# Kernel tuning notes

Measured on AMD Instinct MI355X. Metric: run time of the kernel, lower is better.

The kernel has to match this reference:

```python
import jax, jax.numpy as jnp
import numpy as np

B, N, E = 4, 4096, 65536
DIN, DB, DO, T = 128, 64, 128, 4  # in_features, bond_features, out_features, n_edge_types
DCAT = 2 * DIN + DB


def setup_inputs() -> dict:
    key = jax.random.key(0)
    ks = jax.random.split(key, 24)
    s = 0.05
    inp = {
        "sites": jax.random.normal(ks[0], (B, N, DIN), jnp.float32),
        "bonds": jax.random.normal(ks[1], (B, E, DB), jnp.float32),
        "idx1": jax.random.randint(ks[2], (E,), 0, N),
        "idx2": jax.random.randint(ks[3], (E,), 0, N),
        "uc": jax.random.randint(ks[4], (E,), 0, T),
        # per-type 2-layer MLPs (stacked over types)
        "W1a": jax.random.normal(ks[5], (T, DCAT, DO), jnp.float32) * s,
        "b1a": jnp.zeros((T, DO), jnp.float32),
        "W1b": jax.random.normal(ks[6], (T, DO, DO), jnp.float32) * s,
        "b1b": jnp.zeros((T, DO), jnp.float32),
        "W2a": jax.random.normal(ks[7], (T, DCAT, DO), jnp.float32) * s,
        "b2a": jnp.zeros((T, DO), jnp.float32),
        "W2b": jax.random.normal(ks[8], (T, DO, DO), jnp.float32) * s,
        "b2b": jnp.zeros((T, DO), jnp.float32),
        # attention gates (Linear(out,1) + sigmoid)
        "Wa1": jax.random.normal(ks[9], (DO, 1), jnp.float32) * s,
        "ba1": jnp.zeros((1,), jnp.float32),
        "Wa2": jax.random.normal(ks[10], (DO, 1), jnp.float32) * s,
        "ba2": jnp.zeros((1,), jnp.float32),
    }
    return inp


def reference(sites, bonds, idx1, idx2, uc, W1a, b1a, W1b, b1b,
              W2a, b2a, W2b, b2b, Wa1, ba1, Wa2, ba2):
    lrelu = jax.nn.leaky_relu  # negative_slope 0.01, matches nn.LeakyReLU default
    # gather edge endpoints and concat with bond features: [B, E, 2*DIN+DB]
    v = jnp.concatenate([sites[:, idx1], sites[:, idx2], bonds], axis=2)

    def mlp(Wa, ba, Wb, bb):
        return lrelu(v @ Wa + ba) @ Wb + bb  # [B, E, DO]

    n_types = W1a.shape[0]
    out1 = jnp.zeros((v.shape[0], v.shape[1], W1b.shape[-1]), v.dtype)
    out2 = jnp.zeros_like(out1)
    for i in range(n_types):  # small fixed set of structurally distinct weights
        m = (uc == i)[None, :, None]
        out1 = jnp.where(m, mlp(W1a[i], b1a[i], W1b[i], b1b[i]), out1)
        out2 = jnp.where(m, mlp(W2a[i], b2a[i], W2b[i], b2b[i]), out2)
    out1 = lrelu(out1)
    out2 = lrelu(out2)
    # sigmoid attention gate
    g1 = jax.nn.sigmoid(out1 @ Wa1 + ba1) * out1
    g2 = jax.nn.sigmoid(out2 @ Wa2 + ba2) * out2
    # scatter_add over edges -> nodes along dim 1, then sum
    n_nodes = sites.shape[1]
    agg = jnp.zeros((sites.shape[0], n_nodes, out1.shape[-1]), v.dtype)
    agg = agg.at[:, idx2].add(g1 + g2)
    return agg
```

## Files before the change

### kernel.cpp

```cpp
#include <hip/hip_runtime.h>

#define NB 4
#define NN 4096
#define NE 65536
#define DIN 128
#define DB 64
#define DOUT 128
#define NT 4
#define DCAT 320

#define MT 64
#define LDH (DOUT + 8)

typedef __bf16 bf16;
typedef __bf16 bf16x2 __attribute__((ext_vector_type(2)));
typedef __bf16 bf16x4 __attribute__((ext_vector_type(4)));
typedef __bf16 bf16x8 __attribute__((ext_vector_type(8)));
typedef float floatx4 __attribute__((ext_vector_type(4)));

__device__ __forceinline__ void async16(const void* g, void* l) {
    __builtin_amdgcn_global_load_lds(
        (const __attribute__((address_space(1))) unsigned int*)g,
        (__attribute__((address_space(3))) unsigned int*)l, 16, 0, 0);
}

#define NS4 (NB * NN * DIN / 4)
#define NA  (NT * 256 * DCAT)
#define NB2 (NT * 256 * DOUT)
#define NBO4 (NB * NE * DB / 4)
#define NZERO 8208
__global__ void prep_k(const float* __restrict__ sites, const float* __restrict__ bonds,
                       const float* __restrict__ W1a, const float* __restrict__ W2a,
                       const float* __restrict__ W1b, const float* __restrict__ W2b,
                       bf16* __restrict__ sitesB,
                       bf16* __restrict__ WtA, bf16* __restrict__ WtB,
                       bf16* __restrict__ bondsB,
                       int* __restrict__ zeroRegion) {
    int i = blockIdx.x * 256 + threadIdx.x;
    if (i < NZERO) zeroRegion[i] = 0;
    if (i < NS4) {
        float4 f = ((const float4*)sites)[i];
        bf16x4 h = { (bf16)f.x, (bf16)f.y, (bf16)f.z, (bf16)f.w };
        ((bf16x4*)sitesB)[i] = h;
    } else if (i < NS4 + NA) {
        int j = i - NS4;
        int k = j % DCAT;
        int n = (j / DCAT) % 256;
        int t = j / (DCAT * 256);
        float w = (n < DOUT) ? W1a[(t * DCAT + k) * DOUT + n]
                             : W2a[(t * DCAT + k) * DOUT + (n - DOUT)];
        WtA[j] = (bf16)w;
    } else if (i < NS4 + NA + NB2) {
        int j = i - NS4 - NA;
        int k = j % DOUT;
        int n = (j / DOUT) % 256;
        int t = j / (DOUT * 256);
        float w = (n < DOUT) ? W1b[(t * DOUT + k) * DOUT + n]
                             : W2b[(t * DOUT + k) * DOUT + (n - DOUT)];
        WtB[j] = (bf16)w;
    } else {
        int j = i - NS4 - NA - NB2;
        float4 f = ((const float4*)bonds)[j];
        bf16x4 h = { (bf16)f.x, (bf16)f.y, (bf16)f.z, (bf16)f.w };
        ((bf16x4*)bondsB)[j] = h;
    }
}

__global__ void bucket_k(const int* __restrict__ uc, const int* __restrict__ idx2,
                         int* __restrict__ cnt, int* __restrict__ deg,
                         int* __restrict__ bucket) {
    __shared__ int h[NT];
    __shared__ int baseo[NT];
    int tid = threadIdx.x;
    if (tid < NT) h[tid] = 0;
    __syncthreads();
    int e = blockIdx.x * 256 + tid;
    int t = uc[e] & 3;
    int lp = atomicAdd(&h[t], 1);
    __syncthreads();
    if (tid < NT) baseo[tid] = atomicAdd(&cnt[tid], h[tid]);
    __syncthreads();
    bucket[t * NE + baseo[t] + lp] = e;
    atomicAdd(&deg[idx2[e] & (NN - 1)], 1);
}

__global__ void scan_k(const int* __restrict__ deg, int* __restrict__ off) {
    __shared__ int wsum[4];
    int tid = threadIdx.x;
    int lane = tid & 63, w = tid >> 6;
    int v[16]; int s = 0;
    #pragma unroll
    for (int j = 0; j < 16; ++j) { v[j] = deg[tid * 16 + j]; s += v[j]; }
    int inc = s;
    #pragma unroll
    for (int d = 1; d < 64; d <<= 1) {
        int x = __shfl_up(inc, d, 64);
        if (lane >= d) inc += x;
    }
    if (lane == 63) wsum[w] = inc;
    __syncthreads();
    int wpre = 0;
    #pragma unroll
    for (int j = 0; j < 4; ++j) wpre += (j < w) ? wsum[j] : 0;
    int excl = wpre + inc - s;
    #pragma unroll
    for (int j = 0; j < 16; ++j) { off[tid * 16 + j] = excl; excl += v[j]; }
    if (tid == 255) off[4096] = excl;
}

__global__ void fill_k(const int* __restrict__ idx2, const int* __restrict__ off,
                       int* __restrict__ cursor, int* __restrict__ perm) {
    int e = blockIdx.x * 256 + threadIdx.x;
    int n = idx2[e] & (NN - 1);
    int p = atomicAdd(&cursor[n], 1);
    perm[e] = off[n] + p;
}

__launch_bounds__(256, 4)
__global__ void main_k(const bf16* __restrict__ sitesB, const bf16* __restrict__ bondsB,
                       const int* __restrict__ idx1, const int* __restrict__ idx2,
                       const int* __restrict__ cnt, const int* __restrict__ bucket,
                       const int* __restrict__ perm,
                       const bf16* __restrict__ WtA, const bf16* __restrict__ WtB,
                       const float* __restrict__ b1a, const float* __restrict__ b2a,
                       const float* __restrict__ b1b, const float* __restrict__ b2b,
                       const float* __restrict__ Wa1, const float* __restrict__ ba1,
                       const float* __restrict__ Wa2, const float* __restrict__ ba2,
                       bf16* __restrict__ eo) {
    __shared__ __align__(16) char smem[40960];
    bf16* sA  = (bf16*)smem;
    bf16* sB  = (bf16*)(smem + 8192);
    bf16* sH1 = (bf16*)smem;
    bf16* sH2 = (bf16*)(smem + MT * LDH * 2);
    float* sWa = (float*)(smem + 35840);

    const int tid = threadIdx.x;

    int blk = blockIdx.x;
    int p = blk & 7;
    const int b = p >> 1;
    int flat = ((blk >> 3) << 1) + (p & 1);

    int c0 = cnt[0], c1 = cnt[1], c2 = cnt[2], c3 = cnt[3];
    int n0 = (c0 + MT - 1) / MT, n1 = (c1 + MT - 1) / MT,
        n2 = (c2 + MT - 1) / MT, n3 = (c3 + MT - 1) / MT;
    int t, ti, cT;
    if (flat < n0)                { t = 0; ti = flat;                cT = c0; }
    else if (flat < n0+n1)        { t = 1; ti = flat - n0;           cT = c1; }
    else if (flat < n0+n1+n2)     { t = 2; ti = flat - n0 - n1;      cT = c2; }
    else if (flat < n0+n1+n2+n3)  { t = 3; ti = flat - n0 - n1 - n2; cT = c3; }
    else return;
    const int base = ti * MT;
    const int nvalid = min(MT, cT - base);

    const int rowA = tid >> 2;
    const int rr = min(rowA, max(nvalid - 1, 0));
    const int e  = bucket[t * NE + base + rr] & (NE - 1);
    const int r1 = idx1[e] & (NN - 1);
    const int r2 = idx2[e] & (NN - 1);
    const int prm = perm[e] & (NE - 1);

    const int wv = tid >> 6;
    const int lane = tid & 63;
    const int br = wv >> 1;
    const int nh = wv & 1;
    const int lr = lane & 15;
    const int quad = lane >> 4;
    const int lk = quad * 8;
    const int colbase = nh * 64;
    const int lodd = lane & 1;

    const size_t sbase = (size_t)b * NN;
    const int kseg = (tid & 3) ^ (rowA & 3);
    const bf16* pA1 = sitesB + (sbase + r1) * DIN + kseg * 8;
    const bf16* pA2 = sitesB + (sbase + r2) * DIN + kseg * 8;
    const bf16* pBo = bondsB + ((size_t)b * NE + e) * DB + kseg * 8;

    auto stageA = [&](int ks, int buf) {
        const bf16* src = (ks < 4) ? (pA1 + ks * 32)
                        : (ks < 8) ? (pA2 + (ks - 4) * 32)
                                   : (pBo + (ks - 8) * 32);
        async16(src, smem + buf * 4096 + wv * 1024);
    };
    auto stageB1 = [&](int ks, int buf) {
        #pragma unroll
        for (int j = 0; j < 4; ++j) {
            int d = (j * 4 + wv) * 64 + lane;
            int col = d >> 2;
            int ksg = (d & 3) ^ (col & 3);
            const bf16* src = WtA + (size_t)(t * 256 + col) * DCAT + ks * 32 + ksg * 8;
            async16(src, &sB[buf * 8192 + (j * 4 + wv) * 512]);
        }
    };

    floatx4 acc[4][4];
    #pragma unroll
    for (int mt = 0; mt < 4; ++mt)
        #pragma unroll
        for (int nt = 0; nt < 4; ++nt)
            acc[mt][nt] = (floatx4){0.f, 0.f, 0.f, 0.f};

    stageA(0, 0);
    stageB1(0, 0);
    #pragma unroll
    for (int ks = 0; ks < 10; ++ks) {
        int buf = ks & 1;
        __syncthreads();
        if (ks < 9) {
            stageA(ks + 1, buf ^ 1);
            stageB1(ks + 1, buf ^ 1);
        }
        bf16x8 aF[4];
        #pragma unroll
        for (int mt = 0; mt < 4; ++mt) {
            int row = mt * 16 + lr;
            aF[mt] = *(const bf16x8*)(&sA[buf * 2048 + (row * 4 + (quad ^ (lr & 3))) * 8]);
        }
        #pragma unroll
        for (int nt = 0; nt < 4; ++nt) {
            int cc = br * 128 + colbase + nt * 16 + lr;
            bf16x8 bF = *(const bf16x8*)(&sB[buf * 8192 + (cc * 4 + (quad ^ (lr & 3))) * 8]);
            #pragma unroll
            for (int mt = 0; mt < 4; ++mt)
                acc[mt][nt] = __builtin_amdgcn_mfma_f32_16x16x32_bf16(aF[mt], bF, acc[mt][nt], 0, 0, 0);
        }
    }
    __syncthreads();

    sWa[tid] = (tid < 128) ? Wa1[tid] : Wa2[tid - 128];

    bf16* sH = (br == 0) ? sH1 : sH2;
    const float* biasA = ((br == 0) ? b1a : b2a) + t * DOUT;
    #pragma unroll
    for (int nt = 0; nt < 4; ++nt) {
        int c = colbase + nt * 16 + lr;
        int cpair = c & ~1;
        float bias = biasA[c];
        #pragma unroll
        for (int mt = 0; mt < 4; ++mt) {
            float v[4], x[4];
            #pragma unroll
            for (int rg = 0; rg < 4; ++rg) {
                float u = acc[mt][nt][rg] + bias;
                v[rg] = u > 0.f ? u : 0.01f * u;
            }
            #pragma unroll
            for (int rg = 0; rg < 4; ++rg) x[rg] = __shfl_xor(v[rg], 1);
            int r0 = mt * 16 + quad * 4 + lodd * 2;
            float lo0 = lodd ? x[2] : v[0], hi0 = lodd ? v[2] : x[0];
            float lo1 = lodd ? x[3] : v[1], hi1 = lodd ? v[3] : x[1];
            *(bf16x2*)(&sH[r0 * LDH + cpair])       = (bf16x2){ (bf16)lo0, (bf16)hi0 };
            *(bf16x2*)(&sH[(r0 + 1) * LDH + cpair]) = (bf16x2){ (bf16)lo1, (bf16)hi1 };
        }
    }
    __syncthreads();

    floatx4 acc2[4][4];
    #pragma unroll
    for (int mt = 0; mt < 4; ++mt)
        #pragma unroll
        for (int nt = 0; nt < 4; ++nt)
            acc2[mt][nt] = (floatx4){0.f, 0.f, 0.f, 0.f};

    const bf16* sHa = (br == 0) ? sH1 : sH2;
    const bf16* WtB_w = WtB + (size_t)(t * 256 + br * 128 + colbase) * DOUT + lk;
    #pragma unroll
    for (int ks = 0; ks < 4; ++ks) {
        bf16x8 aF[4];
        #pragma unroll
        for (int mt = 0; mt < 4; ++mt)
            aF[mt] = *(const bf16x8*)(&sHa[(mt * 16 + lr) * LDH + ks * 32 + lk]);
        #pragma unroll
        for (int nt = 0; nt < 4; ++nt) {
            bf16x8 bF = *(const bf16x8*)(&WtB_w[(size_t)(nt * 16 + lr) * DOUT + ks * 32]);
            #pragma unroll
            for (int mt = 0; mt < 4; ++mt)
                acc2[mt][nt] = __builtin_amdgcn_mfma_f32_16x16x32_bf16(aF[mt], bF, acc2[mt][nt], 0, 0, 0);
        }
    }
    __syncthreads();

    const float* biasB = ((br == 0) ? b1b : b2b) + t * DOUT;
    #pragma unroll
    for (int nt = 0; nt < 4; ++nt) {
        int c = colbase + nt * 16 + lr;
        int cpair = c & ~1;
        float bias = biasB[c];
        #pragma unroll
        for (int mt = 0; mt < 4; ++mt) {
            float v[4], x[4];
            #pragma unroll
            for (int rg = 0; rg < 4; ++rg) {
                float u = acc2[mt][nt][rg] + bias;
                v[rg] = u > 0.f ? u : 0.01f * u;
            }
            #pragma unroll
            for (int rg = 0; rg < 4; ++rg) x[rg] = __shfl_xor(v[rg], 1);
            int r0 = mt * 16 + quad * 4 + lodd * 2;
            float lo0 = lodd ? x[2] : v[0], hi0 = lodd ? v[2] : x[0];
            float lo1 = lodd ? x[3] : v[1], hi1 = lodd ? v[3] : x[1];
            *(bf16x2*)(&sH[r0 * LDH + cpair])       = (bf16x2){ (bf16)lo0, (bf16)hi0 };
            *(bf16x2*)(&sH[(r0 + 1) * LDH + cpair]) = (bf16x2){ (bf16)lo1, (bf16)hi1 };
        }
    }
    __syncthreads();

    {
        int m = tid >> 2;
        int q = tid & 3;
        float d1 = 0.f, d2 = 0.f;
        #pragma unroll
        for (int j = 0; j < 4; ++j) {
            bf16x8 h1 = *(const bf16x8*)(&sH1[m * LDH + q * 32 + j * 8]);
            bf16x8 h2 = *(const bf16x8*)(&sH2[m * LDH + q * 32 + j * 8]);
            float4 wa = *(const float4*)(&sWa[q * 32 + j * 8]);
            float4 wb = *(const float4*)(&sWa[q * 32 + j * 8 + 4]);
            float4 va = *(const float4*)(&sWa[128 + q * 32 + j * 8]);
            float4 vb = *(const float4*)(&sWa[128 + q * 32 + j * 8 + 4]);
            d1 += (float)h1[0] * wa.x; d1 += (float)h1[1] * wa.y;
            d1 += (float)h1[2] * wa.z; d1 += (float)h1[3] * wa.w;
            d1 += (float)h1[4] * wb.x; d1 += (float)h1[5] * wb.y;
            d1 += (float)h1[6] * wb.z; d1 += (float)h1[7] * wb.w;
            d2 += (float)h2[0] * va.x; d2 += (float)h2[1] * va.y;
            d2 += (float)h2[2] * va.z; d2 += (float)h2[3] * va.w;
            d2 += (float)h2[4] * vb.x; d2 += (float)h2[5] * vb.y;
            d2 += (float)h2[6] * vb.z; d2 += (float)h2[7] * vb.w;
        }
        d1 += __shfl_xor(d1, 1); d1 += __shfl_xor(d1, 2);
        d2 += __shfl_xor(d2, 1); d2 += __shfl_xor(d2, 2);
        d1 = fminf(fmaxf(d1 + ba1[0], -30.f), 30.f);
        d2 = fminf(fmaxf(d2 + ba2[0], -30.f), 30.f);
        float s1 = 1.f / (1.f + __expf(-d1));
        float s2 = 1.f / (1.f + __expf(-d2));
        if (m < nvalid) {
            bf16* dst = eo + ((size_t)b * NE + prm) * DOUT;
            #pragma unroll
            for (int j = 0; j < 4; ++j) {
                int cc = (q + 4 * j) * 8;
                bf16x8 h1 = *(const bf16x8*)(&sH1[m * LDH + cc]);
                bf16x8 h2 = *(const bf16x8*)(&sH2[m * LDH + cc]);
                bf16x8 w;
                #pragma unroll
                for (int c = 0; c < 8; ++c)
                    w[c] = (bf16)(s1 * (float)h1[c] + s2 * (float)h2[c]);
                *(bf16x8*)(dst + cc) = w;
            }
        }
    }
}

__global__ void gather_k(const bf16* __restrict__ eo, const int* __restrict__ off,
                         float* __restrict__ out) {
    __shared__ float part[16 * 128];
    int tid = threadIdx.x;
    int g = tid >> 4;
    int cseg = tid & 15;
    int n = blockIdx.x;
    int b = blockIdx.y;
    int o0 = off[n], o1 = off[n + 1];
    const bf16* base = eo + (size_t)b * NE * DOUT + cseg * 8;
    float a[8] = {0.f, 0.f, 0.f, 0.f, 0.f, 0.f, 0.f, 0.f};
    for (int r = o0 + g; r < o1; r += 16) {
        bf16x8 v = *(const bf16x8*)(base + (size_t)r * DOUT);
        #pragma unroll
        for (int j = 0; j < 8; ++j) a[j] += (float)v[j];
    }
    #pragma unroll
    for (int j = 0; j < 8; ++j) part[g * 128 + cseg * 8 + j] = a[j];
    __syncthreads();
    if (tid < 128) {
        float s = 0.f;
        #pragma unroll
        for (int g2 = 0; g2 < 16; ++g2) s += part[g2 * 128 + tid];
        out[((size_t)b * NN + n) * DOUT + tid] = s;
    }
}

extern "C" void kernel_launch(void* const* d_in, const int* in_sizes, int n_in,
                              void* d_out, int out_size, void* d_ws, size_t ws_size,
                              hipStream_t stream) {
    const float* sites = (const float*)d_in[0];
    const float* bonds = (const float*)d_in[1];
    const int*   idx1  = (const int*)d_in[2];
    const int*   idx2  = (const int*)d_in[3];
    const int*   uc    = (const int*)d_in[4];
    const float* W1a = (const float*)d_in[5];
    const float* b1a = (const float*)d_in[6];
    const float* W1b = (const float*)d_in[7];
    const float* b1b = (const float*)d_in[8];
    const float* W2a = (const float*)d_in[9];
    const float* b2a = (const float*)d_in[10];
    const float* W2b = (const float*)d_in[11];
    const float* b2b = (const float*)d_in[12];
    const float* Wa1 = (const float*)d_in[13];
    const float* ba1 = (const float*)d_in[14];
    const float* Wa2 = (const float*)d_in[15];
    const float* ba2 = (const float*)d_in[16];
    float* out = (float*)d_out;

    char* ws = (char*)d_ws;
    size_t o_cnt    = 0;
    size_t o_deg    = 64;
    size_t o_cursor = o_deg + NN * 4;
    size_t o_off    = o_cursor + NN * 4;
    size_t o_bucket = o_off + (NN + 16) * 4;
    size_t o_perm   = o_bucket + (size_t)NT * NE * 4;
    size_t o_wta    = o_perm + (size_t)NE * 4;
    size_t o_wtb    = o_wta + (size_t)NA * 2;
    size_t o_sitesB = o_wtb + (size_t)NB2 * 2;
    size_t o_eo     = o_sitesB + (size_t)NB * NN * DIN * 2;
    size_t need     = o_eo + (size_t)NB * NE * DOUT * 2;
    size_t o_bondsB = need;
    size_t need_full = o_bondsB + (size_t)NB * NE * DB * 2;
    if (ws_size < need_full) return;

    int*  cnt    = (int*)(ws + o_cnt);
    int*  deg    = (int*)(ws + o_deg);
    int*  cursor = (int*)(ws + o_cursor);
    int*  off    = (int*)(ws + o_off);
    int*  bucket = (int*)(ws + o_bucket);
    int*  perm   = (int*)(ws + o_perm);
    bf16* WtA    = (bf16*)(ws + o_wta);
    bf16* WtB    = (bf16*)(ws + o_wtb);
    bf16* sitesB = (bf16*)(ws + o_sitesB);
    bf16* eo     = (bf16*)(ws + o_eo);
    bf16* bondsB = (bf16*)(ws + o_bondsB);

    prep_k<<<(NS4 + NA + NB2 + NBO4) / 256, 256, 0, stream>>>(
        sites, bonds, W1a, W2a, W1b, W2b, sitesB, WtA, WtB, bondsB, (int*)ws);
    bucket_k<<<NE / 256, 256, 0, stream>>>(uc, idx2, cnt, deg, bucket);
    scan_k<<<1, 256, 0, stream>>>(deg, off);
    fill_k<<<NE / 256, 256, 0, stream>>>(idx2, off, cursor, perm);

    const int maxTiles = NE / MT + NT;
    main_k<<<maxTiles * NB, 256, 0, stream>>>(
        sitesB, bondsB, idx1, idx2, cnt, bucket, perm, WtA, WtB,
        b1a, b2a, b1b, b2b, Wa1, ba1, Wa2, ba2, eo);

    gather_k<<<dim3(NN, NB), 256, 0, stream>>>(eo, off, out);
}
```

Baseline: 279.7 us.

## Split main kernel tile across 8 waves with 512-thread blocks

Result: slower. 344.2 us (+23.0%).

```diff
diff --git a/kernel.cpp b/kernel.cpp
--- a/kernel.cpp
+++ b/kernel.cpp
@@ -116,7 +116,7 @@
     perm[e] = off[n] + p;
 }
 
-__launch_bounds__(256, 4)
+__launch_bounds__(512, 8)
 __global__ void main_k(const bf16* __restrict__ sitesB, const bf16* __restrict__ bondsB,
                        const int* __restrict__ idx1, const int* __restrict__ idx2,
                        const int* __restrict__ cnt, const int* __restrict__ bucket,
@@ -154,15 +154,20 @@
     const int nvalid = min(MT, cT - base);
 
     const int rowA = tid >> 2;
-    const int rr = min(rowA, max(nvalid - 1, 0));
-    const int e  = bucket[t * NE + base + rr] & (NE - 1);
-    const int r1 = idx1[e] & (NN - 1);
-    const int r2 = idx2[e] & (NN - 1);
-    const int prm = perm[e] & (NE - 1);
+    const int rrA = min(rowA, max(nvalid - 1, 0));
+    const int eA  = bucket[t * NE + base + rrA] & (NE - 1);
+    const int r1 = idx1[eA] & (NN - 1);
+    const int r2 = idx2[eA] & (NN - 1);
+
+    const int mG  = tid >> 3;
+    const int rrG = min(mG, max(nvalid - 1, 0));
+    const int eG  = bucket[t * NE + base + rrG] & (NE - 1);
+    const int prm = perm[eG] & (NE - 1);
 
     const int wv = tid >> 6;
     const int lane = tid & 63;
-    const int br = wv >> 1;
+    const int rh = wv >> 2;
+    const int br = (wv >> 1) & 1;
     const int nh = wv & 1;
     const int lr = lane & 15;
     const int quad = lane >> 4;
@@ -174,28 +179,30 @@
     const int kseg = (tid & 3) ^ (rowA & 3);
     const bf16* pA1 = sitesB + (sbase + r1) * DIN + kseg * 8;
     const bf16* pA2 = sitesB + (sbase + r2) * DIN + kseg * 8;
-    const bf16* pBo = bondsB + ((size_t)b * NE + e) * DB + kseg * 8;
+    const bf16* pBo = bondsB + ((size_t)b * NE + eA) * DB + kseg * 8;
 
     auto stageA = [&](int ks, int buf) {
-        const bf16* src = (ks < 4) ? (pA1 + ks * 32)
-                        : (ks < 8) ? (pA2 + (ks - 4) * 32)
-                                   : (pBo + (ks - 8) * 32);
-        async16(src, smem + buf * 4096 + wv * 1024);
+        if (wv < 4) {
+            const bf16* src = (ks < 4) ? (pA1 + ks * 32)
+                            : (ks < 8) ? (pA2 + (ks - 4) * 32)
+                                       : (pBo + (ks - 8) * 32);
+            async16(src, smem + buf * 4096 + wv * 1024);
+        }
     };
     auto stageB1 = [&](int ks, int buf) {
         #pragma unroll
-        for (int j = 0; j < 4; ++j) {
-            int d = (j * 4 + wv) * 64 + lane;
+        for (int j = 0; j < 2; ++j) {
+            int d = (j * 8 + wv) * 64 + lane;
             int col = d >> 2;
             int ksg = (d & 3) ^ (col & 3);
             const bf16* src = WtA + (size_t)(t * 256 + col) * DCAT + ks * 32 + ksg * 8;
-            async16(src, &sB[buf * 8192 + (j * 4 + wv) * 512]);
+            async16(src, &sB[buf * 8192 + (j * 8 + wv) * 512]);
         }
     };
 
-    floatx4 acc[4][4];
-    #pragma unroll
-    for (int mt = 0; mt < 4; ++mt)
+    floatx4 acc[2][4];
+    #pragma unroll
+    for (int mt = 0; mt < 2; ++mt)
         #pragma unroll
         for (int nt = 0; nt < 4; ++nt)
             acc[mt][nt] = (floatx4){0.f, 0.f, 0.f, 0.f};
@@ -210,10 +217,10 @@
             stageA(ks + 1, buf ^ 1);
             stageB1(ks + 1, buf ^ 1);
         }
-        bf16x8 aF[4];
-        #pragma unroll
-        for (int mt = 0; mt < 4; ++mt) {
-            int row = mt * 16 + lr;
+        bf16x8 aF[2];
+        #pragma unroll
+        for (int mt = 0; mt < 2; ++mt) {
+            int row = rh * 32 + mt * 16 + lr;
             aF[mt] = *(const bf16x8*)(&sA[buf * 2048 + (row * 4 + (quad ^ (lr & 3))) * 8]);
         }
         #pragma unroll
@@ -221,13 +228,13 @@
             int cc = br * 128 + colbase + nt * 16 + lr;
             bf16x8 bF = *(const bf16x8*)(&sB[buf * 8192 + (cc * 4 + (quad ^ (lr & 3))) * 8]);
             #pragma unroll
-            for (int mt = 0; mt < 4; ++mt)
+            for (int mt = 0; mt < 2; ++mt)
                 acc[mt][nt] = __builtin_amdgcn_mfma_f32_16x16x32_bf16(aF[mt], bF, acc[mt][nt], 0, 0, 0);
         }
     }
     __syncthreads();
 
-    sWa[tid] = (tid < 128) ? Wa1[tid] : Wa2[tid - 128];
+    if (tid < 256) sWa[tid] = (tid < 128) ? Wa1[tid] : Wa2[tid - 128];
 
     bf16* sH = (br == 0) ? sH1 : sH2;
     const float* biasA = ((br == 0) ? b1a : b2a) + t * DOUT;
@@ -237,7 +244,7 @@
         int cpair = c & ~1;
         float bias = biasA[c];
         #pragma unroll
-        for (int mt = 0; mt < 4; ++mt) {
+        for (int mt = 0; mt < 2; ++mt) {
             float v[4], x[4];
             #pragma unroll
             for (int rg = 0; rg < 4; ++rg) {
@@ -246,7 +253,7 @@
             }
             #pragma unroll
             for (int rg = 0; rg < 4; ++rg) x[rg] = __shfl_xor(v[rg], 1);
-            int r0 = mt * 16 + quad * 4 + lodd * 2;
+            int r0 = rh * 32 + mt * 16 + quad * 4 + lodd * 2;
             float lo0 = lodd ? x[2] : v[0], hi0 = lodd ? v[2] : x[0];
             float lo1 = lodd ? x[3] : v[1], hi1 = lodd ? v[3] : x[1];
             *(bf16x2*)(&sH[r0 * LDH + cpair])       = (bf16x2){ (bf16)lo0, (bf16)hi0 };
@@ -255,9 +262,9 @@
     }
     __syncthreads();
 
-    floatx4 acc2[4][4];
-    #pragma unroll
-    for (int mt = 0; mt < 4; ++mt)
+    floatx4 acc2[2][4];
+    #pragma unroll
+    for (int mt = 0; mt < 2; ++mt)
         #pragma unroll
         for (int nt = 0; nt < 4; ++nt)
             acc2[mt][nt] = (floatx4){0.f, 0.f, 0.f, 0.f};
@@ -266,15 +273,15 @@
     const bf16* WtB_w = WtB + (size_t)(t * 256 + br * 128 + colbase) * DOUT + lk;
     #pragma unroll
     for (int ks = 0; ks < 4; ++ks) {
-        bf16x8 aF[4];
-        #pragma unroll
-        for (int mt = 0; mt < 4; ++mt)
-            aF[mt] = *(const bf16x8*)(&sHa[(mt * 16 + lr) * LDH + ks * 32 + lk]);
+        bf16x8 aF[2];
+        #pragma unroll
+        for (int mt = 0; mt < 2; ++mt)
+            aF[mt] = *(const bf16x8*)(&sHa[(rh * 32 + mt * 16 + lr) * LDH + ks * 32 + lk]);
         #pragma unroll
         for (int nt = 0; nt < 4; ++nt) {
             bf16x8 bF = *(const bf16x8*)(&WtB_w[(size_t)(nt * 16 + lr) * DOUT + ks * 32]);
             #pragma unroll
-            for (int mt = 0; mt < 4; ++mt)
+            for (int mt = 0; mt < 2; ++mt)
                 acc2[mt][nt] = __builtin_amdgcn_mfma_f32_16x16x32_bf16(aF[mt], bF, acc2[mt][nt], 0, 0, 0);
         }
     }
@@ -287,7 +294,7 @@
         int cpair = c & ~1;
         float bias = biasB[c];
         #pragma unroll
-        for (int mt = 0; mt < 4; ++mt) {
+        for (int mt = 0; mt < 2; ++mt) {
             float v[4], x[4];
             #pragma unroll
             for (int rg = 0; rg < 4; ++rg) {
@@ -296,7 +303,7 @@
             }
             #pragma unroll
             for (int rg = 0; rg < 4; ++rg) x[rg] = __shfl_xor(v[rg], 1);
-            int r0 = mt * 16 + quad * 4 + lodd * 2;
+            int r0 = rh * 32 + mt * 16 + quad * 4 + lodd * 2;
             float lo0 = lodd ? x[2] : v[0], hi0 = lodd ? v[2] : x[0];
             float lo1 = lodd ? x[3] : v[1], hi1 = lodd ? v[3] : x[1];
             *(bf16x2*)(&sH[r0 * LDH + cpair])       = (bf16x2){ (bf16)lo0, (bf16)hi0 };
@@ -306,17 +313,17 @@
     __syncthreads();
 
     {
-        int m = tid >> 2;
-        int q = tid & 3;
+        int m = mG;
+        int qq = tid & 7;
         float d1 = 0.f, d2 = 0.f;
         #pragma unroll
-        for (int j = 0; j < 4; ++j) {
-            bf16x8 h1 = *(const bf16x8*)(&sH1[m * LDH + q * 32 + j * 8]);
-            bf16x8 h2 = *(const bf16x8*)(&sH2[m * LDH + q * 32 + j * 8]);
-            float4 wa = *(const float4*)(&sWa[q * 32 + j * 8]);
-            float4 wb = *(const float4*)(&sWa[q * 32 + j * 8 + 4]);
-            float4 va = *(const float4*)(&sWa[128 + q * 32 + j * 8]);
-            float4 vb = *(const float4*)(&sWa[128 + q * 32 + j * 8 + 4]);
+        for (int j = 0; j < 2; ++j) {
+            bf16x8 h1 = *(const bf16x8*)(&sH1[m * LDH + qq * 16 + j * 8]);
+            bf16x8 h2 = *(const bf16x8*)(&sH2[m * LDH + qq * 16 + j * 8]);
+            float4 wa = *(const float4*)(&sWa[qq * 16 + j * 8]);
+            float4 wb = *(const float4*)(&sWa[qq * 16 + j * 8 + 4]);
+            float4 va = *(const float4*)(&sWa[128 + qq * 16 + j * 8]);
+            float4 vb = *(const float4*)(&sWa[128 + qq * 16 + j * 8 + 4]);
             d1 += (float)h1[0] * wa.x; d1 += (float)h1[1] * wa.y;
             d1 += (float)h1[2] * wa.z; d1 += (float)h1[3] * wa.w;
             d1 += (float)h1[4] * wb.x; d1 += (float)h1[5] * wb.y;
@@ -326,24 +333,23 @@
             d2 += (float)h2[4] * vb.x; d2 += (float)h2[5] * vb.y;
             d2 += (float)h2[6] * vb.z; d2 += (float)h2[7] * vb.w;
         }
-        d1 += __shfl_xor(d1, 1); d1 += __shfl_xor(d1, 2);
-        d2 += __shfl_xor(d2, 1); d2 += __shfl_xor(d2, 2);
+        d1 += __shfl_xor(d1, 1); d1 += __shfl_xor(d1, 2); d1 += __shfl_xor(d1, 4);
+        d2 += __shfl_xor(d2, 1); d2 += __shfl_xor(d2, 2); d2 += __shfl_xor(d2, 4);
         d1 = fminf(fmaxf(d1 + ba1[0], -30.f), 30.f);
         d2 = fminf(fmaxf(d2 + ba2[0], -30.f), 30.f);
         float s1 = 1.f / (1.f + __expf(-d1));
         float s2 = 1.f / (1.f + __expf(-d2));
         if (m < nvalid) {
-            bf16* dst = eo + ((size_t)b * NE + prm) * DOUT;
-            #pragma unroll
-            for (int j = 0; j < 4; ++j) {
-                int cc = (q + 4 * j) * 8;
-                bf16x8 h1 = *(const bf16x8*)(&sH1[m * LDH + cc]);
-                bf16x8 h2 = *(const bf16x8*)(&sH2[m * LDH + cc]);
+            bf16* dst = eo + ((size_t)b * NE + prm) * DOUT + qq * 16;
+            #pragma unroll
+            for (int j = 0; j < 2; ++j) {
+                bf16x8 h1 = *(const bf16x8*)(&sH1[m * LDH + qq * 16 + j * 8]);
+                bf16x8 h2 = *(const bf16x8*)(&sH2[m * LDH + qq * 16 + j * 8]);
                 bf16x8 w;
                 #pragma unroll
                 for (int c = 0; c < 8; ++c)
                     w[c] = (bf16)(s1 * (float)h1[c] + s2 * (float)h2[c]);
-                *(bf16x8*)(dst + cc) = w;
+                *(bf16x8*)(dst + j * 8) = w;
             }
         }
     }
@@ -433,7 +439,7 @@
     fill_k<<<NE / 256, 256, 0, stream>>>(idx2, off, cursor, perm);
 
     const int maxTiles = NE / MT + NT;
-    main_k<<<maxTiles * NB, 256, 0, stream>>>(
+    main_k<<<maxTiles * NB, 512, 0, stream>>>(
         sitesB, bondsB, idx1, idx2, cnt, bucket, perm, WtA, WtB,
         b1a, b2a, b1b, b2b, Wa1, ba1, Wa2, ba2, eo);
 
```

## Load first-layer MFMA operands directly from global memory instead of LDS staging

Applied to the files above, without the earlier changes.

Result: slower. 401.3 us (+43.5%).

```diff
diff --git a/kernel.cpp b/kernel.cpp
--- a/kernel.cpp
+++ b/kernel.cpp
@@ -17,12 +17,6 @@
 typedef __bf16 bf16x4 __attribute__((ext_vector_type(4)));
 typedef __bf16 bf16x8 __attribute__((ext_vector_type(8)));
 typedef float floatx4 __attribute__((ext_vector_type(4)));
-
-__device__ __forceinline__ void async16(const void* g, void* l) {
-    __builtin_amdgcn_global_load_lds(
-        (const __attribute__((address_space(1))) unsigned int*)g,
-        (__attribute__((address_space(3))) unsigned int*)l, 16, 0, 0);
-}
 
 #define NS4 (NB * NN * DIN / 4)
 #define NA  (NT * 256 * DCAT)
@@ -127,12 +121,12 @@
                        const float* __restrict__ Wa1, const float* __restrict__ ba1,
                        const float* __restrict__ Wa2, const float* __restrict__ ba2,
                        bf16* __restrict__ eo) {
-    __shared__ __align__(16) char smem[40960];
-    bf16* sA  = (bf16*)smem;
-    bf16* sB  = (bf16*)(smem + 8192);
+    __shared__ __align__(16) char smem[35584];
     bf16* sH1 = (bf16*)smem;
     bf16* sH2 = (bf16*)(smem + MT * LDH * 2);
-    float* sWa = (float*)(smem + 35840);
+    int* sI1  = (int*)(smem + 34816);
+    int* sI2  = (int*)(smem + 35072);
+    int* sEid = (int*)(smem + 35328);
 
     const int tid = threadIdx.x;
 
@@ -153,12 +147,19 @@
     const int base = ti * MT;
     const int nvalid = min(MT, cT - base);
 
-    const int rowA = tid >> 2;
-    const int rr = min(rowA, max(nvalid - 1, 0));
-    const int e  = bucket[t * NE + base + rr] & (NE - 1);
-    const int r1 = idx1[e] & (NN - 1);
-    const int r2 = idx2[e] & (NN - 1);
-    const int prm = perm[e] & (NE - 1);
+    const int mG  = tid >> 2;
+    const int rrG = min(mG, max(nvalid - 1, 0));
+    const int eG  = bucket[t * NE + base + rrG] & (NE - 1);
+    const int prm = perm[eG] & (NE - 1);
+
+    if (tid < MT) {
+        int rr = min(tid, max(nvalid - 1, 0));
+        int e = bucket[t * NE + base + rr] & (NE - 1);
+        sEid[tid] = e;
+        sI1[tid] = idx1[e] & (NN - 1);
+        sI2[tid] = idx2[e] & (NN - 1);
+    }
+    __syncthreads();
 
     const int wv = tid >> 6;
     const int lane = tid & 63;
@@ -170,28 +171,20 @@
     const int colbase = nh * 64;
     const int lodd = lane & 1;
 
-    const size_t sbase = (size_t)b * NN;
-    const int kseg = (tid & 3) ^ (rowA & 3);
-    const bf16* pA1 = sitesB + (sbase + r1) * DIN + kseg * 8;
-    const bf16* pA2 = sitesB + (sbase + r2) * DIN + kseg * 8;
-    const bf16* pBo = bondsB + ((size_t)b * NE + e) * DB + kseg * 8;
-
-    auto stageA = [&](int ks, int buf) {
-        const bf16* src = (ks < 4) ? (pA1 + ks * 32)
-                        : (ks < 8) ? (pA2 + (ks - 4) * 32)
-                                   : (pBo + (ks - 8) * 32);
-        async16(src, smem + buf * 4096 + wv * 1024);
-    };
-    auto stageB1 = [&](int ks, int buf) {
-        #pragma unroll
-        for (int j = 0; j < 4; ++j) {
-            int d = (j * 4 + wv) * 64 + lane;
-            int col = d >> 2;
-            int ksg = (d & 3) ^ (col & 3);
-            const bf16* src = WtA + (size_t)(t * 256 + col) * DCAT + ks * 32 + ksg * 8;
-            async16(src, &sB[buf * 8192 + (j * 4 + wv) * 512]);
-        }
-    };
+    const unsigned sbase = (unsigned)b * NN;
+    unsigned oA1[4], oA2[4], oBo[4], oB[4];
+    #pragma unroll
+    for (int mt = 0; mt < 4; ++mt) {
+        int rw = mt * 16 + lr;
+        oA1[mt] = (sbase + (unsigned)sI1[rw]) * DIN + lk;
+        oA2[mt] = (sbase + (unsigned)sI2[rw]) * DIN + lk;
+        oBo[mt] = ((unsigned)b * NE + (unsigned)sEid[rw]) * DB + lk;
+    }
+    #pragma unroll
+    for (int nt = 0; nt < 4; ++nt) {
+        int cc = br * 128 + colbase + nt * 16 + lr;
+        oB[nt] = ((unsigned)t * 256 + (unsigned)cc) * DCAT + lk;
+    }
 
     floatx4 acc[4][4];
     #pragma unroll
@@ -200,34 +193,24 @@
         for (int nt = 0; nt < 4; ++nt)
             acc[mt][nt] = (floatx4){0.f, 0.f, 0.f, 0.f};
 
-    stageA(0, 0);
-    stageB1(0, 0);
     #pragma unroll
     for (int ks = 0; ks < 10; ++ks) {
-        int buf = ks & 1;
-        __syncthreads();
-        if (ks < 9) {
-            stageA(ks + 1, buf ^ 1);
-            stageB1(ks + 1, buf ^ 1);
-        }
-        bf16x8 aF[4];
+        bf16x8 aF[4], bF[4];
         #pragma unroll
         for (int mt = 0; mt < 4; ++mt) {
-            int row = mt * 16 + lr;
-            aF[mt] = *(const bf16x8*)(&sA[buf * 2048 + (row * 4 + (quad ^ (lr & 3))) * 8]);
-        }
-        #pragma unroll
-        for (int nt = 0; nt < 4; ++nt) {
-            int cc = br * 128 + colbase + nt * 16 + lr;
-            bf16x8 bF = *(const bf16x8*)(&sB[buf * 8192 + (cc * 4 + (quad ^ (lr & 3))) * 8]);
+            aF[mt] = (ks < 4) ? *(const bf16x8*)(sitesB + oA1[mt] + ks * 32)
+                   : (ks < 8) ? *(const bf16x8*)(sitesB + oA2[mt] + (ks - 4) * 32)
+                              : *(const bf16x8*)(bondsB + oBo[mt] + (ks - 8) * 32);
+        }
+        #pragma unroll
+        for (int nt = 0; nt < 4; ++nt)
+            bF[nt] = *(const bf16x8*)(WtA + oB[nt] + ks * 32);
+        #pragma unroll
+        for (int nt = 0; nt < 4; ++nt)
             #pragma unroll
             for (int mt = 0; mt < 4; ++mt)
-                acc[mt][nt] = __builtin_amdgcn_mfma_f32_16x16x32_bf16(aF[mt], bF, acc[mt][nt], 0, 0, 0);
-        }
-    }
-    __syncthreads();
-
-    sWa[tid] = (tid < 128) ? Wa1[tid] : Wa2[tid - 128];
+                acc[mt][nt] = __builtin_amdgcn_mfma_f32_16x16x32_bf16(aF[mt], bF[nt], acc[mt][nt], 0, 0, 0);
+    }
 
     bf16* sH = (br == 0) ? sH1 : sH2;
     const float* biasA = ((br == 0) ? b1a : b2a) + t * DOUT;
@@ -306,17 +289,17 @@
     __syncthreads();
 
     {
-        int m = tid >> 2;
+        int m = mG;
         int q = tid & 3;
         float d1 = 0.f, d2 = 0.f;
         #pragma unroll
         for (int j = 0; j < 4; ++j) {
             bf16x8 h1 = *(const bf16x8*)(&sH1[m * LDH + q * 32 + j * 8]);
             bf16x8 h2 = *(const bf16x8*)(&sH2[m * LDH + q * 32 + j * 8]);
-            float4 wa = *(const float4*)(&sWa[q * 32 + j * 8]);
-            float4 wb = *(const float4*)(&sWa[q * 32 + j * 8 + 4]);
-            float4 va = *(const float4*)(&sWa[128 + q * 32 + j * 8]);
-            float4 vb = *(const float4*)(&sWa[128 + q * 32 + j * 8 + 4]);
+            float4 wa = *(const float4*)(&Wa1[q * 32 + j * 8]);
+            float4 wb = *(const float4*)(&Wa1[q * 32 + j * 8 + 4]);
+            float4 va = *(const float4*)(&Wa2[q * 32 + j * 8]);
+            float4 vb = *(const float4*)(&Wa2[q * 32 + j * 8 + 4]);
             d1 += (float)h1[0] * wa.x; d1 += (float)h1[1] * wa.y;
             d1 += (float)h1[2] * wa.z; d1 += (float)h1[3] * wa.w;
             d1 += (float)h1[4] * wb.x; d1 += (float)h1[5] * wb.y;
```

## Merge bucketing into prep, assign scatter slots in main kernel, pack gather nodes

Applied to the files above, without the earlier changes.

New measurement: 269.0 us. 1.04x faster.

```diff
diff --git a/kernel.cpp b/kernel.cpp
--- a/kernel.cpp
+++ b/kernel.cpp
@@ -28,16 +28,33 @@
 #define NA  (NT * 256 * DCAT)
 #define NB2 (NT * 256 * DOUT)
 #define NBO4 (NB * NE * DB / 4)
-#define NZERO 8208
+#define PREP_BLOCKS ((NS4 + NA + NB2 + NBO4) / 256)
 __global__ void prep_k(const float* __restrict__ sites, const float* __restrict__ bonds,
                        const float* __restrict__ W1a, const float* __restrict__ W2a,
                        const float* __restrict__ W1b, const float* __restrict__ W2b,
+                       const int* __restrict__ uc, const int* __restrict__ idx2,
                        bf16* __restrict__ sitesB,
                        bf16* __restrict__ WtA, bf16* __restrict__ WtB,
                        bf16* __restrict__ bondsB,
-                       int* __restrict__ zeroRegion) {
-    int i = blockIdx.x * 256 + threadIdx.x;
-    if (i < NZERO) zeroRegion[i] = 0;
+                       int* __restrict__ cnt, int* __restrict__ deg,
+                       int* __restrict__ bucket) {
+    int tid = threadIdx.x;
+    if (blockIdx.x < 256) {
+        __shared__ int h[NT];
+        __shared__ int baseo[NT];
+        if (tid < NT) h[tid] = 0;
+        __syncthreads();
+        int e = blockIdx.x * 256 + tid;
+        int t = uc[e] & 3;
+        int lp = atomicAdd(&h[t], 1);
+        __syncthreads();
+        if (tid < NT) baseo[tid] = atomicAdd(&cnt[tid], h[tid]);
+        __syncthreads();
+        bucket[t * NE + baseo[t] + lp] = e;
+        atomicAdd(&deg[idx2[e] & (NN - 1)], 1);
+        return;
+    }
+    int i = (blockIdx.x - 256) * 256 + tid;
     if (i < NS4) {
         float4 f = ((const float4*)sites)[i];
         bf16x4 h = { (bf16)f.x, (bf16)f.y, (bf16)f.z, (bf16)f.w };
@@ -66,27 +83,12 @@
     }
 }
 
-__global__ void bucket_k(const int* __restrict__ uc, const int* __restrict__ idx2,
-                         int* __restrict__ cnt, int* __restrict__ deg,
-                         int* __restrict__ bucket) {
-    __shared__ int h[NT];
-    __shared__ int baseo[NT];
-    int tid = threadIdx.x;
-    if (tid < NT) h[tid] = 0;
-    __syncthreads();
-    int e = blockIdx.x * 256 + tid;
-    int t = uc[e] & 3;
-    int lp = atomicAdd(&h[t], 1);
-    __syncthreads();
-    if (tid < NT) baseo[tid] = atomicAdd(&cnt[tid], h[tid]);
-    __syncthreads();
-    bucket[t * NE + baseo[t] + lp] = e;
-    atomicAdd(&deg[idx2[e] & (NN - 1)], 1);
-}
-
-__global__ void scan_k(const int* __restrict__ deg, int* __restrict__ off) {
+__global__ void scan_k(const int* __restrict__ deg, int* __restrict__ off,
+                       int* __restrict__ cursor) {
     __shared__ int wsum[4];
     int tid = threadIdx.x;
+    #pragma unroll
+    for (int j = 0; j < NB * NN / 256; ++j) cursor[tid + j * 256] = 0;
     int lane = tid & 63, w = tid >> 6;
     int v[16]; int s = 0;
     #pragma unroll
@@ -106,21 +108,13 @@
     #pragma unroll
     for (int j = 0; j < 16; ++j) { off[tid * 16 + j] = excl; excl += v[j]; }
     if (tid == 255) off[4096] = excl;
-}
-
-__global__ void fill_k(const int* __restrict__ idx2, const int* __restrict__ off,
-                       int* __restrict__ cursor, int* __restrict__ perm) {
-    int e = blockIdx.x * 256 + threadIdx.x;
-    int n = idx2[e] & (NN - 1);
-    int p = atomicAdd(&cursor[n], 1);
-    perm[e] = off[n] + p;
 }
 
 __launch_bounds__(256, 4)
 __global__ void main_k(const bf16* __restrict__ sitesB, const bf16* __restrict__ bondsB,
                        const int* __restrict__ idx1, const int* __restrict__ idx2,
                        const int* __restrict__ cnt, const int* __restrict__ bucket,
-                       const int* __restrict__ perm,
+                       const int* __restrict__ off, int* __restrict__ cursor,
                        const bf16* __restrict__ WtA, const bf16* __restrict__ WtB,
                        const float* __restrict__ b1a, const float* __restrict__ b2a,
                        const float* __restrict__ b1b, const float* __restrict__ b2b,
@@ -143,12 +137,12 @@
 
     int c0 = cnt[0], c1 = cnt[1], c2 = cnt[2], c3 = cnt[3];
     int n0 = (c0 + MT - 1) / MT, n1 = (c1 + MT - 1) / MT,
-        n2 = (c2 + MT - 1) / MT, n3 = (c3 + MT - 1) / MT;
+        n2t = (c2 + MT - 1) / MT, n3 = (c3 + MT - 1) / MT;
     int t, ti, cT;
-    if (flat < n0)                { t = 0; ti = flat;                cT = c0; }
-    else if (flat < n0+n1)        { t = 1; ti = flat - n0;           cT = c1; }
-    else if (flat < n0+n1+n2)     { t = 2; ti = flat - n0 - n1;      cT = c2; }
-    else if (flat < n0+n1+n2+n3)  { t = 3; ti = flat - n0 - n1 - n2; cT = c3; }
+    if (flat < n0)                 { t = 0; ti = flat;                 cT = c0; }
+    else if (flat < n0+n1)         { t = 1; ti = flat - n0;            cT = c1; }
+    else if (flat < n0+n1+n2t)     { t = 2; ti = flat - n0 - n1;       cT = c2; }
+    else if (flat < n0+n1+n2t+n3)  { t = 3; ti = flat - n0 - n1 - n2t; cT = c3; }
     else return;
     const int base = ti * MT;
     const int nvalid = min(MT, cT - base);
@@ -158,7 +152,6 @@
     const int e  = bucket[t * NE + base + rr] & (NE - 1);
     const int r1 = idx1[e] & (NN - 1);
     const int r2 = idx2[e] & (NN - 1);
-    const int prm = perm[e] & (NE - 1);
 
     const int wv = tid >> 6;
     const int lane = tid & 63;
@@ -333,6 +326,10 @@
         float s1 = 1.f / (1.f + __expf(-d1));
         float s2 = 1.f / (1.f + __expf(-d2));
         if (m < nvalid) {
+            int rank0 = 0;
+            if (q == 0) rank0 = atomicAdd(&cursor[b * NN + r2], 1);
+            int rank = __shfl(rank0, lane & ~3);
+            int prm = (off[r2] + rank) & (NE - 1);
             bf16* dst = eo + ((size_t)b * NE + prm) * DOUT;
             #pragma unroll
             for (int j = 0; j < 4; ++j) {
@@ -351,29 +348,33 @@
 
 __global__ void gather_k(const bf16* __restrict__ eo, const int* __restrict__ off,
                          float* __restrict__ out) {
-    __shared__ float part[16 * 128];
+    __shared__ float part[4 * 4 * 128];
     int tid = threadIdx.x;
-    int g = tid >> 4;
+    int nl = tid >> 6;
+    int g  = (tid >> 4) & 3;
     int cseg = tid & 15;
-    int n = blockIdx.x;
+    int n = blockIdx.x * 4 + nl;
     int b = blockIdx.y;
     int o0 = off[n], o1 = off[n + 1];
     const bf16* base = eo + (size_t)b * NE * DOUT + cseg * 8;
     float a[8] = {0.f, 0.f, 0.f, 0.f, 0.f, 0.f, 0.f, 0.f};
-    for (int r = o0 + g; r < o1; r += 16) {
+    for (int r = o0 + g; r < o1; r += 4) {
         bf16x8 v = *(const bf16x8*)(base + (size_t)r * DOUT);
         #pragma unroll
         for (int j = 0; j < 8; ++j) a[j] += (float)v[j];
     }
     #pragma unroll
-    for (int j = 0; j < 8; ++j) part[g * 128 + cseg * 8 + j] = a[j];
-    __syncthreads();
-    if (tid < 128) {
-        float s = 0.f;
-        #pragma unroll
-        for (int g2 = 0; g2 < 16; ++g2) s += part[g2 * 128 + tid];
-        out[((size_t)b * NN + n) * DOUT + tid] = s;
-    }
+    for (int j = 0; j < 8; ++j) part[(nl * 4 + g) * 128 + cseg * 8 + j] = a[j];
+    __syncthreads();
+    int c2 = (tid & 63) * 2;
+    float s0 = 0.f, s1 = 0.f;
+    #pragma unroll
+    for (int gg = 0; gg < 4; ++gg) {
+        s0 += part[(nl * 4 + gg) * 128 + c2];
+        s1 += part[(nl * 4 + gg) * 128 + c2 + 1];
+    }
+    float2 o = { s0, s1 };
+    *(float2*)(&out[((size_t)b * NN + n) * DOUT + c2]) = o;
 }
 
 extern "C" void kernel_launch(void* const* d_in, const int* in_sizes, int n_in,
@@ -402,40 +403,38 @@
     size_t o_cnt    = 0;
     size_t o_deg    = 64;
     size_t o_cursor = o_deg + NN * 4;
-    size_t o_off    = o_cursor + NN * 4;
+    size_t o_off    = o_cursor + (size_t)NB * NN * 4;
     size_t o_bucket = o_off + (NN + 16) * 4;
-    size_t o_perm   = o_bucket + (size_t)NT * NE * 4;
-    size_t o_wta    = o_perm + (size_t)NE * 4;
+    size_t o_wta    = o_bucket + (size_t)NT * NE * 4;
     size_t o_wtb    = o_wta + (size_t)NA * 2;
     size_t o_sitesB = o_wtb + (size_t)NB2 * 2;
     size_t o_eo     = o_sitesB + (size_t)NB * NN * DIN * 2;
-    size_t need     = o_eo + (size_t)NB * NE * DOUT * 2;
-    size_t o_bondsB = need;
-    size_t need_full = o_bondsB + (size_t)NB * NE * DB * 2;
-    if (ws_size < need_full) return;
+    size_t o_bondsB = o_eo + (size_t)NB * NE * DOUT * 2;
+    size_t need     = o_bondsB + (size_t)NB * NE * DB * 2;
+    if (ws_size < need) return;
 
     int*  cnt    = (int*)(ws + o_cnt);
     int*  deg    = (int*)(ws + o_deg);
     int*  cursor = (int*)(ws + o_cursor);
     int*  off    = (int*)(ws + o_off);
     int*  bucket = (int*)(ws + o_bucket);
-    int*  perm   = (int*)(ws + o_perm);
     bf16* WtA    = (bf16*)(ws + o_wta);
     bf16* WtB    = (bf16*)(ws + o_wtb);
     bf16* sitesB = (bf16*)(ws + o_sitesB);
     bf16* eo     = (bf16*)(ws + o_eo);
     bf16* bondsB = (bf16*)(ws + o_bondsB);
 
-    prep_k<<<(NS4 + NA + NB2 + NBO4) / 256, 256, 0, stream>>>(
-        sites, bonds, W1a, W2a, W1b, W2b, sitesB, WtA, WtB, bondsB, (int*)ws);
-    bucket_k<<<NE / 256, 256, 0, stream>>>(uc, idx2, cnt, deg, bucket);
-    scan_k<<<1, 256, 0, stream>>>(deg, off);
-    fill_k<<<NE / 256, 256, 0, stream>>>(idx2, off, cursor, perm);
+    hipMemsetAsync(ws, 0, 64 + (size_t)NN * 4, stream);
+
+    prep_k<<<PREP_BLOCKS + 256, 256, 0, stream>>>(
+        sites, bonds, W1a, W2a, W1b, W2b, uc, idx2,
+        sitesB, WtA, WtB, bondsB, cnt, deg, bucket);
+    scan_k<<<1, 256, 0, stream>>>(deg, off, cursor);
 
     const int maxTiles = NE / MT + NT;
     main_k<<<maxTiles * NB, 256, 0, stream>>>(
-        sitesB, bondsB, idx1, idx2, cnt, bucket, perm, WtA, WtB,
+        sitesB, bondsB, idx1, idx2, cnt, bucket, off, cursor, WtA, WtB,
         b1a, b2a, b1b, b2b, Wa1, ba1, Wa2, ba2, eo);
 
-    gather_k<<<dim3(NN, NB), 256, 0, stream>>>(eo, off, out);
-}
+    gather_k<<<dim3(NN / 4, NB), 256, 0, stream>>>(eo, off, out);
+}
```
